# Optimization experiments

Hardware: AMD Instinct MI355X
Metric: run time of the kernel (lower is better)

Reference implementation:

```python
import jax, jax.numpy as jnp
import numpy as np


def setup_inputs() -> dict:
    key = jax.random.key(0)
    k1, k2 = jax.random.split(key)
    # x stacks (real, imag) along dim 0: (2, B, C, G, H, W)
    x = jax.random.normal(k1, (2, 8, 512, 4, 32, 32), dtype=jnp.float32)
    # gamma is a learned scalar parameter (torch inits to 0; randomized here for a non-trivial path)
    gamma = jax.random.normal(k2, (1,), dtype=jnp.float32) * 0.1
    return {"x": x, "gamma": gamma}


def reference(x, gamma):
    xr, xi = x[0], x[1]                      # (B, C, G, H, W) real / imag parts
    B, C, G, H, W = xr.shape
    N = G * H * W
    qr = xr.reshape(B, C, N)                 # proj_query == proj_value (gp is None)
    qi = xi.reshape(B, C, N)

    # energy = q @ q^T (complex, no conjugation), shape (B, C, C)
    er = jnp.einsum('bcn,bdn->bcd', qr, qr) - jnp.einsum('bcn,bdn->bcd', qi, qi)
    ei = jnp.einsum('bcn,bdn->bcd', qr, qi) + jnp.einsum('bcn,bdn->bcd', qi, qr)

    # energy_new = complex(max(re), max(im)) - energy  (max over last dim, broadcast)
    er2 = jnp.max(er, axis=-1, keepdims=True) - er
    ei2 = jnp.max(ei, axis=-1, keepdims=True) - ei

    # SoftmaxCmplx: softmax over squared magnitude, output is real
    attention = jax.nn.softmax(er2 * er2 + ei2 * ei2, axis=-1)   # (B, C, C)

    # out = attention @ value (attention real, value complex)
    outr = jnp.einsum('bcd,bdn->bcn', attention, qr).reshape(B, C, G, H, W)
    outi = jnp.einsum('bcd,bdn->bcn', attention, qi).reshape(B, C, G, H, W)

    g = gamma[0]
    # cmplx(real, imag) -> stack along dim 0
    return jnp.stack([g * outr + xr, g * outi + xi], axis=0)
```

## Files before the change

kernel.cpp:

```cpp
#include <hip/hip_runtime.h>
#include <hip/hip_bf16.h>

#define B_ 8
#define C_ 512
#define N_ 4096
#define BK 32
#define NSPLIT 8
#define KCH (N_ / NSPLIT)
static const size_t PS = (size_t)B_ * C_ * C_;

typedef __bf16 bf16x8 __attribute__((ext_vector_type(8)));
typedef float f32x4 __attribute__((ext_vector_type(4)));

__device__ __constant__ unsigned char JCI[36] = {
    0,0,0,0,0,0,0,0, 1,1,1,1,1,1,1, 2,2,2,2,2,2, 3,3,3,3,3, 4,4,4,4, 5,5,5, 6,6, 7};
__device__ __constant__ unsigned char JDJ[36] = {
    0,1,2,3,4,5,6,7, 1,2,3,4,5,6,7, 2,3,4,5,6,7, 3,4,5,6,7, 4,5,6,7, 5,6,7, 6,7, 7};

__device__ __forceinline__ f32x4 mfma16(bf16x8 a, bf16x8 b, f32x4 c) {
    return __builtin_amdgcn_mfma_f32_16x16x32_bf16(a, b, c, 0, 0, 0);
}

__device__ __forceinline__ unsigned cvtpk_bf16(float lo, float hi) {
    unsigned r;
    asm("v_cvt_pk_bf16_f32 %0, %1, %2" : "=v"(r) : "v"(lo), "v"(hi));
    return r;
}

__device__ __forceinline__ void cvt_store4(const f32x4 v, __bf16* hp, __bf16* lp) {
    const unsigned u0 = __float_as_uint(v[0]), u1 = __float_as_uint(v[1]);
    const unsigned u2 = __float_as_uint(v[2]), u3 = __float_as_uint(v[3]);
    uint2 h, l;
    h.x = __builtin_amdgcn_perm(u1, u0, 0x07060302u);
    h.y = __builtin_amdgcn_perm(u3, u2, 0x07060302u);
    l.x = cvtpk_bf16(v[0] - __uint_as_float(u0 & 0xFFFF0000u),
                     v[1] - __uint_as_float(u1 & 0xFFFF0000u));
    l.y = cvtpk_bf16(v[2] - __uint_as_float(u2 & 0xFFFF0000u),
                     v[3] - __uint_as_float(u3 & 0xFFFF0000u));
    *(uint2*)hp = h;
    *(uint2*)lp = l;
}

__global__ __launch_bounds__(256, 3) void energy_kernel(const float* __restrict__ x,
                                                        float* __restrict__ pbuf) {
    __shared__ __align__(16) __bf16 Ah[64][40], Al[64][40], Chs[64][40], Cls[64][40];
    __shared__ __align__(16) __bf16 Bh[64][40], Bl[64][40], Dh[64][40], Dl[64][40];
    const int b = blockIdx.z, sp = blockIdx.y;
    const int cbase = JCI[blockIdx.x] * 64, dbase = JDJ[blockIdx.x] * 64;
    const int t = threadIdx.x, lane = t & 63, wave = t >> 6;
    const int m = lane & 15, quad = lane >> 4;
    const int wr = wave >> 1, wc = wave & 1;

    const float* qr = x + (size_t)b * C_ * N_;
    const float* qi = qr + (size_t)B_ * C_ * N_;
    const int kbase = sp * KCH;

    const int s_row = t >> 2, s_k = (t & 3) * 8;
    const float* agr = qr + (size_t)(cbase + s_row) * N_ + kbase + s_k;
    const float* agi = qi + (size_t)(cbase + s_row) * N_ + kbase + s_k;
    const float* bgr = qr + (size_t)(dbase + s_row) * N_ + kbase + s_k;
    const float* bgi = qi + (size_t)(dbase + s_row) * N_ + kbase + s_k;

    f32x4 accRR[2][2] = {}, accII[2][2] = {}, accEI[2][2] = {};

    for (int k0 = 0; k0 < KCH; k0 += BK) {
        f32x4 va[2], vc[2], vb[2], vd[2];
#pragma unroll
        for (int u = 0; u < 2; ++u) {
            va[u] = *(const f32x4*)(agr + k0 + u * 4);
            vc[u] = *(const f32x4*)(agi + k0 + u * 4);
            vb[u] = *(const f32x4*)(bgr + k0 + u * 4);
            vd[u] = *(const f32x4*)(bgi + k0 + u * 4);
        }
        __syncthreads();
#pragma unroll
        for (int u = 0; u < 2; ++u) {
            cvt_store4(va[u], &Ah[s_row][s_k + u * 4], &Al[s_row][s_k + u * 4]);
            cvt_store4(vc[u], &Chs[s_row][s_k + u * 4], &Cls[s_row][s_k + u * 4]);
            cvt_store4(vb[u], &Bh[s_row][s_k + u * 4], &Bl[s_row][s_k + u * 4]);
            cvt_store4(vd[u], &Dh[s_row][s_k + u * 4], &Dl[s_row][s_k + u * 4]);
        }
        __syncthreads();

        bf16x8 fBh[2], fBl[2], fDh[2], fDl[2];
#pragma unroll
        for (int j = 0; j < 2; ++j) {
            const int row = wc * 32 + j * 16 + m;
            fBh[j] = *(const bf16x8*)&Bh[row][quad * 8];
            fBl[j] = *(const bf16x8*)&Bl[row][quad * 8];
            fDh[j] = *(const bf16x8*)&Dh[row][quad * 8];
            fDl[j] = *(const bf16x8*)&Dl[row][quad * 8];
        }
#pragma unroll
        for (int i = 0; i < 2; ++i) {
            const int row = wr * 32 + i * 16 + m;
            const bf16x8 fAh = *(const bf16x8*)&Ah[row][quad * 8];
            const bf16x8 fAl = *(const bf16x8*)&Al[row][quad * 8];
            const bf16x8 fCh = *(const bf16x8*)&Chs[row][quad * 8];
            const bf16x8 fCl = *(const bf16x8*)&Cls[row][quad * 8];
#pragma unroll
            for (int j = 0; j < 2; ++j) {
                accRR[i][j] = mfma16(fAh, fBh[j], accRR[i][j]);
                accRR[i][j] = mfma16(fAh, fBl[j], accRR[i][j]);
                accRR[i][j] = mfma16(fAl, fBh[j], accRR[i][j]);
                accII[i][j] = mfma16(fCh, fDh[j], accII[i][j]);
                accII[i][j] = mfma16(fCh, fDl[j], accII[i][j]);
                accII[i][j] = mfma16(fCl, fDh[j], accII[i][j]);
                accEI[i][j] = mfma16(fAh, fDh[j], accEI[i][j]);
                accEI[i][j] = mfma16(fAh, fDl[j], accEI[i][j]);
                accEI[i][j] = mfma16(fAl, fDh[j], accEI[i][j]);
                accEI[i][j] = mfma16(fCh, fBh[j], accEI[i][j]);
                accEI[i][j] = mfma16(fCh, fBl[j], accEI[i][j]);
                accEI[i][j] = mfma16(fCl, fBh[j], accEI[i][j]);
            }
        }
    }

    float* per = pbuf + (size_t)(2 * sp) * PS + (size_t)b * C_ * C_;
    float* pei = per + PS;
#pragma unroll
    for (int i = 0; i < 2; ++i)
#pragma unroll
        for (int j = 0; j < 2; ++j) {
            const int c0 = cbase + wr * 32 + i * 16 + quad * 4;
            const int d = dbase + wc * 32 + j * 16 + m;
            const f32x4 e = accRR[i][j] - accII[i][j];
            const f32x4 f = accEI[i][j];
#pragma unroll
            for (int r = 0; r < 4; ++r) {
                per[(size_t)(c0 + r) * C_ + d] = e[r];
                pei[(size_t)(c0 + r) * C_ + d] = f[r];
            }
            *(f32x4*)(per + (size_t)d * C_ + c0) = e;
            *(f32x4*)(pei + (size_t)d * C_ + c0) = f;
        }
}

__device__ __forceinline__ float waveMax(float v) {
#pragma unroll
    for (int off = 32; off > 0; off >>= 1) v = fmaxf(v, __shfl_xor(v, off));
    return v;
}
__device__ __forceinline__ float waveSum(float v) {
#pragma unroll
    for (int off = 32; off > 0; off >>= 1) v += __shfl_xor(v, off);
    return v;
}

__global__ __launch_bounds__(256) void softmax_kernel(const float* __restrict__ pbuf,
                                                      __bf16* __restrict__ att) {
    __shared__ float buf[4];
    const int b = blockIdx.y, c = blockIdx.x, t = threadIdx.x;
    const int wave = t >> 6, lane = t & 63;
    const size_t rbase = ((size_t)(b * C_ + c)) * C_;

    float er0 = 0.f, er1 = 0.f, ei0 = 0.f, ei1 = 0.f;
#pragma unroll
    for (int s = 0; s < NSPLIT; ++s) {
        const float* per = pbuf + (size_t)(2 * s) * PS;
        const float* pei = per + PS;
        er0 += per[rbase + t];
        er1 += per[rbase + t + 256];
        ei0 += pei[rbase + t];
        ei1 += pei[rbase + t + 256];
    }

    float v = waveMax(fmaxf(er0, er1));
    if (lane == 0) buf[wave] = v;
    __syncthreads();
    const float mer = fmaxf(fmaxf(buf[0], buf[1]), fmaxf(buf[2], buf[3]));
    __syncthreads();

    v = waveMax(fmaxf(ei0, ei1));
    if (lane == 0) buf[wave] = v;
    __syncthreads();
    const float mei = fmaxf(fmaxf(buf[0], buf[1]), fmaxf(buf[2], buf[3]));
    __syncthreads();

    const float a0 = mer - er0, c0 = mei - ei0;
    const float a1 = mer - er1, c1 = mei - ei1;
    const float t0 = a0 * a0 + c0 * c0;
    const float t1 = a1 * a1 + c1 * c1;

    v = waveMax(fmaxf(t0, t1));
    if (lane == 0) buf[wave] = v;
    __syncthreads();
    const float mt = fmaxf(fmaxf(buf[0], buf[1]), fmaxf(buf[2], buf[3]));
    __syncthreads();

    const float e0 = expf(t0 - mt), e1 = expf(t1 - mt);
    v = waveSum(e0 + e1);
    if (lane == 0) buf[wave] = v;
    __syncthreads();
    const float s = buf[0] + buf[1] + buf[2] + buf[3];
    const float inv = 1.0f / s;

    att[rbase + t] = (__bf16)(e0 * inv);
    att[rbase + t + 256] = (__bf16)(e1 * inv);
}

__global__ __launch_bounds__(256, 2) void out_kernel(const float* __restrict__ x,
                                                     const __bf16* __restrict__ att,
                                                     const float* __restrict__ gamma,
                                                     float* __restrict__ out) {
    __shared__ __align__(16) unsigned Lr[64 * 20];
    __shared__ __align__(16) unsigned Li[64 * 20];
    const int b = blockIdx.z, ct = blockIdx.y, nt = blockIdx.x;
    const int t = threadIdx.x, lane = t & 63, wave = t >> 6;
    const int m = lane & 15, quad = lane >> 4;

    const float* qr = x + (size_t)b * C_ * N_;
    const float* qi = qr + (size_t)B_ * C_ * N_;
    const int cbase = ct * 256;
    const __bf16* arow = att + ((size_t)(b * C_ + cbase + wave * 16 + m)) * C_ + quad * 8;

    const int kp = t & 15;
    const int n4 = (t >> 4) * 4;
    const int n0 = nt * 64;

    f32x4 accr[4][4] = {}, acci[4][4] = {};
    f32x4 pr0, pr1, pi0, pi1;
    bf16x8 pa[4];

#define LOADO(kk)                                                                \
    {                                                                            \
        pr0 = *(const f32x4*)(qr + (size_t)((kk) + 2 * kp) * N_ + n0 + n4);      \
        pr1 = *(const f32x4*)(qr + (size_t)((kk) + 2 * kp + 1) * N_ + n0 + n4);  \
        pi0 = *(const f32x4*)(qi + (size_t)((kk) + 2 * kp) * N_ + n0 + n4);      \
        pi1 = *(const f32x4*)(qi + (size_t)((kk) + 2 * kp + 1) * N_ + n0 + n4);  \
        _Pragma("unroll") for (int h = 0; h < 4; ++h)                            \
            pa[h] = *(const bf16x8*)(arow + (size_t)(h * 64) * C_ + (kk));       \
    }

    LOADO(0);
    for (int kk = 0; kk < C_; kk += 32) {
        const f32x4 r0 = pr0, r1 = pr1, i0 = pi0, i1 = pi1;
        bf16x8 a[4];
#pragma unroll
        for (int h = 0; h < 4; ++h) a[h] = pa[h];
        __syncthreads();
#pragma unroll
        for (int u = 0; u < 4; ++u) {
            Lr[(n4 + u) * 20 + kp] = cvtpk_bf16(r0[u], r1[u]);
            Li[(n4 + u) * 20 + kp] = cvtpk_bf16(i0[u], i1[u]);
        }
        __syncthreads();

        const int kn = (kk + 32 < C_) ? kk + 32 : 0;
        LOADO(kn);
#pragma unroll
        for (int s = 0; s < 4; ++s) {
            const bf16x8 br = *(const bf16x8*)(&Lr[(s * 16 + m) * 20 + quad * 4]);
            const bf16x8 bi = *(const bf16x8*)(&Li[(s * 16 + m) * 20 + quad * 4]);
#pragma unroll
            for (int h = 0; h < 4; ++h) {
                accr[h][s] = mfma16(a[h], br, accr[h][s]);
                acci[h][s] = mfma16(a[h], bi, acci[h][s]);
            }
        }
    }
#undef LOADO

    const float g = gamma[0];
    float* outr = out + (size_t)b * C_ * N_;
    float* outi = outr + (size_t)B_ * C_ * N_;
#pragma unroll
    for (int h = 0; h < 4; ++h)
#pragma unroll
        for (int s = 0; s < 4; ++s)
#pragma unroll
            for (int r = 0; r < 4; ++r) {
                const int cc = cbase + h * 64 + wave * 16 + quad * 4 + r;
                const int nn = n0 + s * 16 + m;
                const size_t ix = (size_t)cc * N_ + nn;
                outr[ix] = g * accr[h][s][r] + qr[ix];
                outi[ix] = g * acci[h][s][r] + qi[ix];
            }
}

extern "C" void kernel_launch(void* const* d_in, const int* in_sizes, int n_in,
                              void* d_out, int out_size, void* d_ws, size_t ws_size,
                              hipStream_t stream) {
    const float* x = (const float*)d_in[0];
    const float* gamma = (const float*)d_in[1];
    float* out = (float*)d_out;

    float* pbuf = out;
    __bf16* att = (__bf16*)d_ws;

    energy_kernel<<<dim3(36, NSPLIT, B_), 256, 0, stream>>>(x, pbuf);
    softmax_kernel<<<dim3(C_, B_), 256, 0, stream>>>(pbuf, att);
    out_kernel<<<dim3(64, 2, 8), 256, 0, stream>>>(x, att, gamma, out);
}
```

Measured before the change: 443.1 us.

## Swizzle energy block order, vectorize softmax, double-buffer LDS in output GEMM

The energy kernel launches as a flat grid whose block index is remapped so that consecutive hardware blocks spread across XCD groups, aiming for better L2 locality on shared rows. The softmax kernel reads partial sums as float2, stores packed bf16 pairs, merges the two max reductions and drops redundant barriers. The output kernel double-buffers its LDS staging so only one barrier per k-step is needed, overlapping global loads with MFMA work. The cost is extra LDS in the output kernel, which may affect occupancy.

Measured after the change: 422.8 us. 1.05x faster.

```diff
diff --git a/kernel.cpp b/kernel.cpp
--- a/kernel.cpp
+++ b/kernel.cpp
@@ -45,8 +45,13 @@
                                                         float* __restrict__ pbuf) {
     __shared__ __align__(16) __bf16 Ah[64][40], Al[64][40], Chs[64][40], Cls[64][40];
     __shared__ __align__(16) __bf16 Bh[64][40], Bl[64][40], Dh[64][40], Dl[64][40];
-    const int b = blockIdx.z, sp = blockIdx.y;
-    const int cbase = JCI[blockIdx.x] * 64, dbase = JDJ[blockIdx.x] * 64;
+    const int bid = blockIdx.x;
+    const int logical = (bid & 7) * 288 + (bid >> 3);
+    const int job = logical % 36;
+    const int grp = logical / 36;
+    const int sp = grp & 7, b = grp >> 3;
+
+    const int cbase = JCI[job] * 64, dbase = JDJ[job] * 64;
     const int t = threadIdx.x, lane = t & 63, wave = t >> 6;
     const int m = lane & 15, quad = lane >> 4;
     const int wr = wave >> 1, wc = wave & 1;
@@ -149,62 +154,57 @@
 
 __global__ __launch_bounds__(256) void softmax_kernel(const float* __restrict__ pbuf,
                                                       __bf16* __restrict__ att) {
-    __shared__ float buf[4];
+    __shared__ float bufA[4][2];
+    __shared__ float bufB[4];
+    __shared__ float bufC[4];
     const int b = blockIdx.y, c = blockIdx.x, t = threadIdx.x;
     const int wave = t >> 6, lane = t & 63;
     const size_t rbase = ((size_t)(b * C_ + c)) * C_;
 
-    float er0 = 0.f, er1 = 0.f, ei0 = 0.f, ei1 = 0.f;
+    float erx = 0.f, ery = 0.f, eix = 0.f, eiy = 0.f;
 #pragma unroll
     for (int s = 0; s < NSPLIT; ++s) {
         const float* per = pbuf + (size_t)(2 * s) * PS;
         const float* pei = per + PS;
-        er0 += per[rbase + t];
-        er1 += per[rbase + t + 256];
-        ei0 += pei[rbase + t];
-        ei1 += pei[rbase + t + 256];
-    }
-
-    float v = waveMax(fmaxf(er0, er1));
-    if (lane == 0) buf[wave] = v;
+        const float2 er = *(const float2*)(per + rbase + 2 * t);
+        const float2 ei = *(const float2*)(pei + rbase + 2 * t);
+        erx += er.x; ery += er.y;
+        eix += ei.x; eiy += ei.y;
+    }
+
+    float vr = waveMax(fmaxf(erx, ery));
+    float vi = waveMax(fmaxf(eix, eiy));
+    if (lane == 0) { bufA[wave][0] = vr; bufA[wave][1] = vi; }
     __syncthreads();
-    const float mer = fmaxf(fmaxf(buf[0], buf[1]), fmaxf(buf[2], buf[3]));
-    __syncthreads();
-
-    v = waveMax(fmaxf(ei0, ei1));
-    if (lane == 0) buf[wave] = v;
-    __syncthreads();
-    const float mei = fmaxf(fmaxf(buf[0], buf[1]), fmaxf(buf[2], buf[3]));
-    __syncthreads();
-
-    const float a0 = mer - er0, c0 = mei - ei0;
-    const float a1 = mer - er1, c1 = mei - ei1;
+    const float mer = fmaxf(fmaxf(bufA[0][0], bufA[1][0]), fmaxf(bufA[2][0], bufA[3][0]));
+    const float mei = fmaxf(fmaxf(bufA[0][1], bufA[1][1]), fmaxf(bufA[2][1], bufA[3][1]));
+
+    const float a0 = mer - erx, c0 = mei - eix;
+    const float a1 = mer - ery, c1 = mei - eiy;
     const float t0 = a0 * a0 + c0 * c0;
     const float t1 = a1 * a1 + c1 * c1;
 
-    v = waveMax(fmaxf(t0, t1));
-    if (lane == 0) buf[wave] = v;
+    float v = waveMax(fmaxf(t0, t1));
+    if (lane == 0) bufB[wave] = v;
     __syncthreads();
-    const float mt = fmaxf(fmaxf(buf[0], buf[1]), fmaxf(buf[2], buf[3]));
-    __syncthreads();
+    const float mt = fmaxf(fmaxf(bufB[0], bufB[1]), fmaxf(bufB[2], bufB[3]));
 
     const float e0 = expf(t0 - mt), e1 = expf(t1 - mt);
     v = waveSum(e0 + e1);
-    if (lane == 0) buf[wave] = v;
+    if (lane == 0) bufC[wave] = v;
     __syncthreads();
-    const float s = buf[0] + buf[1] + buf[2] + buf[3];
+    const float s = bufC[0] + bufC[1] + bufC[2] + bufC[3];
     const float inv = 1.0f / s;
 
-    att[rbase + t] = (__bf16)(e0 * inv);
-    att[rbase + t + 256] = (__bf16)(e1 * inv);
+    *(unsigned*)(att + rbase + 2 * t) = cvtpk_bf16(e0 * inv, e1 * inv);
 }
 
 __global__ __launch_bounds__(256, 2) void out_kernel(const float* __restrict__ x,
                                                      const __bf16* __restrict__ att,
                                                      const float* __restrict__ gamma,
                                                      float* __restrict__ out) {
-    __shared__ __align__(16) unsigned Lr[64 * 20];
-    __shared__ __align__(16) unsigned Li[64 * 20];
+    __shared__ __align__(16) unsigned Lr[2][64 * 20];
+    __shared__ __align__(16) unsigned Li[2][64 * 20];
     const int b = blockIdx.z, ct = blockIdx.y, nt = blockIdx.x;
     const int t = threadIdx.x, lane = t & 63, wave = t >> 6;
     const int m = lane & 15, quad = lane >> 4;
@@ -233,31 +233,31 @@
     }
 
     LOADO(0);
+    int cur = 0;
     for (int kk = 0; kk < C_; kk += 32) {
         const f32x4 r0 = pr0, r1 = pr1, i0 = pi0, i1 = pi1;
         bf16x8 a[4];
 #pragma unroll
         for (int h = 0; h < 4; ++h) a[h] = pa[h];
-        __syncthreads();
 #pragma unroll
         for (int u = 0; u < 4; ++u) {
-            Lr[(n4 + u) * 20 + kp] = cvtpk_bf16(r0[u], r1[u]);
-            Li[(n4 + u) * 20 + kp] = cvtpk_bf16(i0[u], i1[u]);
-        }
-        __syncthreads();
-
+            Lr[cur][(n4 + u) * 20 + kp] = cvtpk_bf16(r0[u], r1[u]);
+            Li[cur][(n4 + u) * 20 + kp] = cvtpk_bf16(i0[u], i1[u]);
+        }
         const int kn = (kk + 32 < C_) ? kk + 32 : 0;
         LOADO(kn);
+        __syncthreads();
 #pragma unroll
         for (int s = 0; s < 4; ++s) {
-            const bf16x8 br = *(const bf16x8*)(&Lr[(s * 16 + m) * 20 + quad * 4]);
-            const bf16x8 bi = *(const bf16x8*)(&Li[(s * 16 + m) * 20 + quad * 4]);
+            const bf16x8 br = *(const bf16x8*)(&Lr[cur][(s * 16 + m) * 20 + quad * 4]);
+            const bf16x8 bi = *(const bf16x8*)(&Li[cur][(s * 16 + m) * 20 + quad * 4]);
 #pragma unroll
             for (int h = 0; h < 4; ++h) {
                 accr[h][s] = mfma16(a[h], br, accr[h][s]);
                 acci[h][s] = mfma16(a[h], bi, acci[h][s]);
             }
         }
+        cur ^= 1;
     }
 #undef LOADO
 
@@ -288,7 +288,7 @@
     float* pbuf = out;
     __bf16* att = (__bf16*)d_ws;
 
-    energy_kernel<<<dim3(36, NSPLIT, B_), 256, 0, stream>>>(x, pbuf);
+    energy_kernel<<<dim3(36 * NSPLIT * B_), 256, 0, stream>>>(x, pbuf);
     softmax_kernel<<<dim3(C_, B_), 256, 0, stream>>>(pbuf, att);
     out_kernel<<<dim3(64, 2, 8), 256, 0, stream>>>(x, att, gamma, out);
 }
```
